# Kernel tuning notes

Measured on AMD Instinct MI355X. Metric: run time of the kernel, lower is better.

The kernel has to match this reference:

```python
import jax, jax.numpy as jnp
import numpy as np

B, T, TQ, E = 32, 200, 50, 64
P, C = 128, 64
BN_EPS = 1e-6
DICE_EPS = 1e-6


def _bn(x, g, b, m, v):
    # inference-mode batch norm over last axis
    return (x - m) * jax.lax.rsqrt(v + BN_EPS) * g + b


def _dice(x, alpha, m, v):
    # Dice activation: p = sigmoid(BN(x, no scale/shift)); out = p*x + alpha*(1-p)*x
    p = jax.nn.sigmoid((x - m) * jax.lax.rsqrt(v + DICE_EPS))
    return p * x + alpha * (1.0 - p) * x


def setup_inputs() -> dict:
    key = jax.random.key(0)
    ks = jax.random.split(key, 16)
    def g(k, shape, scale=0.05):
        return jax.random.normal(k, shape, dtype=jnp.float32) * scale
    inp = {
        "user_behavior": jax.random.normal(ks[0], (B, T, E), dtype=jnp.float32),
        "items": jax.random.normal(ks[1], (B, TQ, E), dtype=jnp.float32),
        "user_profile": jax.random.normal(ks[2], (B, P), dtype=jnp.float32),
        "context": jax.random.normal(ks[3], (B, C), dtype=jnp.float32),
        # attention MLP
        "W1": g(ks[4], (4 * E, 36)), "b1": jnp.zeros((36,), jnp.float32),
        "dice_alpha": jnp.zeros((36,), jnp.float32),
        "dice_mean": jnp.zeros((36,), jnp.float32),
        "dice_var": jnp.ones((36,), jnp.float32),
        "W2": g(ks[5], (36, 1)), "b2": jnp.zeros((1,), jnp.float32),
        # trunk MLP (input dim E+P+C = 256)
        "bn1_g": jnp.ones((E + P + C,), jnp.float32), "bn1_b": jnp.zeros((E + P + C,), jnp.float32),
        "bn1_m": jnp.zeros((E + P + C,), jnp.float32), "bn1_v": jnp.ones((E + P + C,), jnp.float32),
        "Wm1": g(ks[6], (E + P + C, 256)), "bm1": jnp.zeros((256,), jnp.float32),
        "bn2_g": jnp.ones((256,), jnp.float32), "bn2_b": jnp.zeros((256,), jnp.float32),
        "bn2_m": jnp.zeros((256,), jnp.float32), "bn2_v": jnp.ones((256,), jnp.float32),
        "Wm2": g(ks[7], (256, 128)), "bm2": jnp.zeros((128,), jnp.float32),
        "bn3_g": jnp.ones((128,), jnp.float32), "bn3_b": jnp.zeros((128,), jnp.float32),
        "bn3_m": jnp.zeros((128,), jnp.float32), "bn3_v": jnp.ones((128,), jnp.float32),
        "Wm3": g(ks[8], (128, 64)), "bm3": jnp.zeros((64,), jnp.float32),
    }
    return inp


def reference(user_behavior, items, user_profile, context,
              W1, b1, dice_alpha, dice_mean, dice_var, W2, b2,
              bn1_g, bn1_b, bn1_m, bn1_v, Wm1, bm1,
              bn2_g, bn2_b, bn2_m, bn2_v, Wm2, bm2,
              bn3_g, bn3_b, bn3_m, bn3_v, Wm3, bm3):
    b, t, e = user_behavior.shape
    tq = items.shape[1]
    # tile/concat cross product: (B, T', T, 4E)
    q = jnp.broadcast_to(user_behavior[:, None, :, :], (b, tq, t, e))
    k = jnp.broadcast_to(items[:, :, None, :], (b, tq, t, e))
    x = jnp.concatenate([q, k, q - k, q * k], axis=-1)
    x = jnp.einsum('btsf,fu->btsu', x, W1) + b1
    x = _dice(x, dice_alpha, dice_mean, dice_var)
    weight = (jnp.einsum('btsu,uo->btso', x, W2) + b2)[..., 0]  # (B, T', T)
    # weighted sum over history: (B, T', E)
    interest = jnp.einsum('bts,bse->bte', weight, user_behavior)
    # trunk MLP (dropout is identity at inference)
    up = jnp.broadcast_to(user_profile[:, None, :], (b, tq, user_profile.shape[-1]))
    cx = jnp.broadcast_to(context[:, None, :], (b, tq, context.shape[-1]))
    h = jnp.concatenate([interest, up, cx], axis=-1)
    h = _bn(h, bn1_g, bn1_b, bn1_m, bn1_v)
    h = jax.nn.relu(h @ Wm1 + bm1)
    h = _bn(h, bn2_g, bn2_b, bn2_m, bn2_v)
    h = jax.nn.relu(h @ Wm2 + bm2)
    h = _bn(h, bn3_g, bn3_b, bn3_m, bn3_v)
    h = jax.nn.relu(h @ Wm3 + bm3)
    return h
```

## Files before the change

### kernel.cpp

```cpp
#include <hip/hip_runtime.h>
#include <hip/hip_bf16.h>
#include <math.h>

#define NB  32
#define NT  200
#define NTQ 50
#define NE  64
#define NP  128
#define NC  64
#define NU  36
#define NROW (NB * NTQ)

typedef __attribute__((ext_vector_type(8))) short bf8;
typedef __attribute__((ext_vector_type(4))) float f4;

#define WM1F_OFF 0
#define WM2F_OFF 65536
#define WM3F_OFF 98304
#define W1F_OFF  106496
#define HH_OFF   115712

#define ATTN_BLOCKS 1600
#define PACK_ELEMS  (65536 + 32768 + 8192)
#define PACK_BLOCKS (PACK_ELEMS / 256)

__device__ __forceinline__ short f2bf(float x) {
    __hip_bfloat16 h = __float2bfloat16(x);
    return __builtin_bit_cast(short, h);
}
__device__ __forceinline__ float bf2f(short s) {
    unsigned u = ((unsigned)(unsigned short)s) << 16;
    return __builtin_bit_cast(float, u);
}

__global__ __launch_bounds__(256) void prep_w1(const float* __restrict__ W1,
                                               short* __restrict__ w1f) {
    int j = blockIdx.x * 256 + threadIdx.x;
    int i = j & 7, lane = (j >> 3) & 63, tile = j >> 9;
    int ks = tile % 6, nt = tile / 6;
    int kk = ks * 32 + 8 * (lane >> 4) + i;
    int n  = nt * 16 + (lane & 15);
    float v = 0.f;
    if (n < NU) {
        if (kk < 128) {
            v = W1[(128 + kk) * NU + n];
            if (kk < 64) v += W1[kk * NU + n];
        } else {
            v = W1[(kk - 64) * NU + n] - W1[kk * NU + n];
        }
    }
    w1f[j] = f2bf(v);
}

__device__ __forceinline__ void pack_frag(int j, const float* W, int N, int ksc, short* dst) {
    int i    = j & 7;
    int lane = (j >> 3) & 63;
    int tile = j >> 9;
    int ks = tile % ksc;
    int nt = tile / ksc;
    int k = ks * 32 + 8 * (lane >> 4) + i;
    int n = nt * 16 + (lane & 15);
    dst[j] = f2bf(W[k * N + n]);
}

struct AParams {
    const float *ub, *it, *b1, *W2, *b2, *da, *dm, *dv;
    const float *bn1_g, *bn1_b, *bn1_m, *bn1_v;
    const float *Wm1, *Wm2, *Wm3;
    const short *w1f;
    short *wm1f, *wm2f, *wm3f;
    short* Hh;
};

__global__ __launch_bounds__(256) void attn(AParams P) {
    const int bid = blockIdx.x;
    const int tid = threadIdx.x;

    if (bid >= ATTN_BLOCKS) {
        int j = (bid - ATTN_BLOCKS) * 256 + tid;
        if (j < 65536) { pack_frag(j, P.Wm1, 256, 8, P.wm1f); return; }
        j -= 65536;
        if (j < 32768) { pack_frag(j, P.Wm2, 128, 8, P.wm2f); return; }
        j -= 32768;
        pack_frag(j, P.Wm3, 64, 4, P.wm3f);
        return;
    }

    __shared__ float w_s[NT];
    __shared__ float red_s[256];

    const int l = tid & 63, w = tid >> 6;
    const int tq = bid % NTQ, b = bid / NTQ;
    const int ul = l & 15;

    const bf8* wf = (const bf8*)P.w1f;

    bf8 bfr[3][4];
    #pragma unroll
    for (int nt = 0; nt < 3; ++nt)
        #pragma unroll
        for (int ks = 0; ks < 4; ++ks)
            bfr[nt][ks] = wf[(nt * 6 + ks) * 64 + l];

    bf8 ak[2];
    {
        const float* itr = P.it + ((size_t)b * NTQ + tq) * NE;
        #pragma unroll
        for (int ks = 0; ks < 2; ++ks) {
            int e0 = ks * 32 + 8 * (l >> 4);
            f4 v0 = *(const f4*)(itr + e0);
            f4 v1 = *(const f4*)(itr + e0 + 4);
            #pragma unroll
            for (int i = 0; i < 4; ++i) {
                ak[ks][i]     = f2bf(v0[i]);
                ak[ks][4 + i] = f2bf(v1[i]);
            }
        }
    }

    f4 acc0[3];
    #pragma unroll
    for (int nt = 0; nt < 3; ++nt) {
        bf8 kb0 = wf[(nt * 6 + 4) * 64 + l];
        bf8 kb1 = wf[(nt * 6 + 5) * 64 + l];
        f4 z; z[0]=0.f; z[1]=0.f; z[2]=0.f; z[3]=0.f;
        z = __builtin_amdgcn_mfma_f32_16x16x32_bf16(ak[0], kb0, z, 0, 0, 0);
        z = __builtin_amdgcn_mfma_f32_16x16x32_bf16(ak[1], kb1, z, 0, 0, 0);
        acc0[nt] = z;
    }

    float b1v[3], dmv[3], drs[3], dav[3], w2v[3];
    #pragma unroll
    for (int nt = 0; nt < 3; ++nt) {
        int u = nt * 16 + ul;
        bool v = (u < NU);
        int uc = v ? u : (NU - 1);
        b1v[nt] = P.b1[uc];
        dmv[nt] = P.dm[uc];
        drs[nt] = rsqrtf(P.dv[uc] + 1e-6f);
        dav[nt] = P.da[uc];
        w2v[nt] = v ? P.W2[uc] : 0.f;
    }
    const float b2s = P.b2[0];

    for (int tt = w; tt < 13; tt += 4) {
        const int t0 = tt * 16;
        const int tA = t0 + (l & 15);

        bf8 aq[2], ap[2];
        if (tA < NT) {
            const float* ubr = P.ub + ((size_t)b * NT + tA) * NE;
            #pragma unroll
            for (int ks = 0; ks < 2; ++ks) {
                int e0 = ks * 32 + 8 * (l >> 4);
                f4 u0 = *(const f4*)(ubr + e0);
                f4 u1 = *(const f4*)(ubr + e0 + 4);
                #pragma unroll
                for (int i = 0; i < 4; ++i) {
                    float q0 = u0[i], q1 = u1[i];
                    aq[ks][i]     = f2bf(q0);
                    aq[ks][4 + i] = f2bf(q1);
                    ap[ks][i]     = f2bf(q0 * bf2f(ak[ks][i]));
                    ap[ks][4 + i] = f2bf(q1 * bf2f(ak[ks][4 + i]));
                }
            }
        } else {
            #pragma unroll
            for (int ks = 0; ks < 2; ++ks)
                #pragma unroll
                for (int i = 0; i < 8; ++i) { aq[ks][i] = 0; ap[ks][i] = 0; }
        }

        f4 acc[3];
        #pragma unroll
        for (int nt = 0; nt < 3; ++nt) acc[nt] = acc0[nt];
        #pragma unroll
        for (int nt = 0; nt < 3; ++nt) {
            acc[nt] = __builtin_amdgcn_mfma_f32_16x16x32_bf16(aq[0], bfr[nt][0], acc[nt], 0, 0, 0);
            acc[nt] = __builtin_amdgcn_mfma_f32_16x16x32_bf16(aq[1], bfr[nt][1], acc[nt], 0, 0, 0);
            acc[nt] = __builtin_amdgcn_mfma_f32_16x16x32_bf16(ap[0], bfr[nt][2], acc[nt], 0, 0, 0);
            acc[nt] = __builtin_amdgcn_mfma_f32_16x16x32_bf16(ap[1], bfr[nt][3], acc[nt], 0, 0, 0);
        }

        const int tD = t0 + 4 * (l >> 4);
        #pragma unroll
        for (int i = 0; i < 4; ++i) {
            int t = tD + i;
            bool tv = (t < NT);
            float val = 0.f;
            #pragma unroll
            for (int nt = 0; nt < 3; ++nt) {
                float x = acc[nt][i] + b1v[nt];
                float z = (x - dmv[nt]) * drs[nt];
                float p = 1.f / (1.f + __expf(-z));
                val += x * (dav[nt] + p * (1.f - dav[nt])) * w2v[nt];
            }
            val += __shfl_xor(val, 1);
            val += __shfl_xor(val, 2);
            val += __shfl_xor(val, 4);
            val += __shfl_xor(val, 8);
            if (ul == 0 && tv) w_s[t] = val + b2s;
        }
    }
    __syncthreads();

    {
        const int e = tid & 63, g = tid >> 6;
        const float* ubb = P.ub + (size_t)b * NT * NE;
        float s = 0.f;
        #pragma unroll 5
        for (int t = g * 50; t < g * 50 + 50; ++t)
            s = fmaf(w_s[t], ubb[t * NE + e], s);
        red_s[tid] = s;
    }
    __syncthreads();
    if (tid < 64) {
        float tot = red_s[tid] + red_s[64 + tid] + red_s[128 + tid] + red_s[192 + tid];
        float hn = (tot - P.bn1_m[tid]) * rsqrtf(P.bn1_v[tid] + 1e-6f) * P.bn1_g[tid] + P.bn1_b[tid];
        P.Hh[((size_t)b * NTQ + tq) * 64 + tid] = f2bf(hn);
    }
}

struct TParams {
    const short *Hh, *wm1f, *wm2f, *wm3f;
    const float *up, *cx;
    const float *bn1_g, *bn1_b, *bn1_m, *bn1_v;
    const float *bm1, *bm2, *bm3;
    const float *bn2_g, *bn2_b, *bn2_m, *bn2_v;
    const float *bn3_g, *bn3_b, *bn3_m, *bn3_v;
    float* out;
};

#define LSTR 264

__global__ __launch_bounds__(256) void trunk(TParams P) {
    __shared__ short Ha[16 * LSTR];
    __shared__ short Hb[16 * LSTR];

    const int tid = threadIdx.x;
    const int l = tid & 63, w = tid >> 6;
    const int row0 = blockIdx.x * 16;

    {
        const bf8* src = (const bf8*)(P.Hh + (size_t)row0 * 64);
        for (int ch = tid; ch < 16 * 8; ch += 256) {
            int r = ch >> 3, c8 = ch & 7;
            *(bf8*)&Ha[r * LSTR + c8 * 8] = src[r * 8 + c8];
        }
    }
    for (int ch = tid; ch < 16 * 192; ch += 256) {
        int r = ch / 192, c = ch % 192;
        int col = 64 + c;
        int b = (row0 + r) / NTQ;
        float val = (c < NP) ? P.up[b * NP + c] : P.cx[b * NC + (c - NP)];
        float hn = (val - P.bn1_m[col]) * rsqrtf(P.bn1_v[col] + 1e-6f)
                   * P.bn1_g[col] + P.bn1_b[col];
        Ha[r * LSTR + col] = f2bf(hn);
    }
    __syncthreads();

    const int ar = l & 15;
    const int rl = 4 * (l >> 4);
    const int nl = l & 15;

    {
        bf8 a[8];
        #pragma unroll
        for (int ks = 0; ks < 8; ++ks)
            a[ks] = *(const bf8*)&Ha[ar * LSTR + ks * 32 + 8 * (l >> 4)];
        const bf8* wf = (const bf8*)P.wm1f;
        #pragma unroll
        for (int nt0 = 0; nt0 < 4; ++nt0) {
            int nt = w * 4 + nt0;
            f4 acc; acc[0]=0.f; acc[1]=0.f; acc[2]=0.f; acc[3]=0.f;
            #pragma unroll
            for (int ks = 0; ks < 8; ++ks)
                acc = __builtin_amdgcn_mfma_f32_16x16x32_bf16(a[ks], wf[(nt * 8 + ks) * 64 + l], acc, 0, 0, 0);
            int n = nt * 16 + nl;
            float g1 = P.bn2_g[n] * rsqrtf(P.bn2_v[n] + 1e-6f);
            float c1 = P.bn2_b[n] - P.bn2_m[n] * g1;
            float bias = P.bm1[n];
            #pragma unroll
            for (int i = 0; i < 4; ++i) {
                float v = fmaxf(acc[i] + bias, 0.f);
                Hb[(rl + i) * LSTR + n] = f2bf(v * g1 + c1);
            }
        }
    }
    __syncthreads();

    {
        bf8 a[8];
        #pragma unroll
        for (int ks = 0; ks < 8; ++ks)
            a[ks] = *(const bf8*)&Hb[ar * LSTR + ks * 32 + 8 * (l >> 4)];
        const bf8* wf = (const bf8*)P.wm2f;
        #pragma unroll
        for (int nt0 = 0; nt0 < 2; ++nt0) {
            int nt = w * 2 + nt0;
            f4 acc; acc[0]=0.f; acc[1]=0.f; acc[2]=0.f; acc[3]=0.f;
            #pragma unroll
            for (int ks = 0; ks < 8; ++ks)
                acc = __builtin_amdgcn_mfma_f32_16x16x32_bf16(a[ks], wf[(nt * 8 + ks) * 64 + l], acc, 0, 0, 0);
            int n = nt * 16 + nl;
            float g1 = P.bn3_g[n] * rsqrtf(P.bn3_v[n] + 1e-6f);
            float c1 = P.bn3_b[n] - P.bn3_m[n] * g1;
            float bias = P.bm2[n];
            #pragma unroll
            for (int i = 0; i < 4; ++i) {
                float v = fmaxf(acc[i] + bias, 0.f);
                Ha[(rl + i) * LSTR + n] = f2bf(v * g1 + c1);
            }
        }
    }
    __syncthreads();

    {
        bf8 a[4];
        #pragma unroll
        for (int ks = 0; ks < 4; ++ks)
            a[ks] = *(const bf8*)&Ha[ar * LSTR + ks * 32 + 8 * (l >> 4)];
        const bf8* wf = (const bf8*)P.wm3f;
        {
            int nt = w;
            f4 acc; acc[0]=0.f; acc[1]=0.f; acc[2]=0.f; acc[3]=0.f;
            #pragma unroll
            for (int ks = 0; ks < 4; ++ks)
                acc = __builtin_amdgcn_mfma_f32_16x16x32_bf16(a[ks], wf[(nt * 4 + ks) * 64 + l], acc, 0, 0, 0);
            int n = nt * 16 + nl;
            float bias = P.bm3[n];
            #pragma unroll
            for (int i = 0; i < 4; ++i)
                P.out[(size_t)(row0 + rl + i) * 64 + n] = fmaxf(acc[i] + bias, 0.f);
        }
    }
}

extern "C" void kernel_launch(void* const* d_in, const int* in_sizes, int n_in,
                              void* d_out, int out_size, void* d_ws, size_t ws_size,
                              hipStream_t stream) {
    (void)in_sizes; (void)n_in; (void)out_size; (void)ws_size;

    const float* ub         = (const float*)d_in[0];
    const float* it         = (const float*)d_in[1];
    const float* up         = (const float*)d_in[2];
    const float* cx         = (const float*)d_in[3];
    const float* W1         = (const float*)d_in[4];
    const float* b1         = (const float*)d_in[5];
    const float* dice_alpha = (const float*)d_in[6];
    const float* dice_mean  = (const float*)d_in[7];
    const float* dice_var   = (const float*)d_in[8];
    const float* W2         = (const float*)d_in[9];
    const float* b2         = (const float*)d_in[10];
    const float* bn1_g      = (const float*)d_in[11];
    const float* bn1_b      = (const float*)d_in[12];
    const float* bn1_m      = (const float*)d_in[13];
    const float* bn1_v      = (const float*)d_in[14];
    const float* Wm1        = (const float*)d_in[15];
    const float* bm1        = (const float*)d_in[16];
    const float* bn2_g      = (const float*)d_in[17];
    const float* bn2_b      = (const float*)d_in[18];
    const float* bn2_m      = (const float*)d_in[19];
    const float* bn2_v      = (const float*)d_in[20];
    const float* Wm2        = (const float*)d_in[21];
    const float* bm2        = (const float*)d_in[22];
    const float* bn3_g      = (const float*)d_in[23];
    const float* bn3_b      = (const float*)d_in[24];
    const float* bn3_m      = (const float*)d_in[25];
    const float* bn3_v      = (const float*)d_in[26];
    const float* Wm3        = (const float*)d_in[27];
    const float* bm3        = (const float*)d_in[28];

    short* wsb  = (short*)d_ws;
    short* wm1f = wsb + WM1F_OFF;
    short* wm2f = wsb + WM2F_OFF;
    short* wm3f = wsb + WM3F_OFF;
    short* w1f  = wsb + W1F_OFF;
    short* Hh   = wsb + HH_OFF;

    prep_w1<<<36, 256, 0, stream>>>(W1, w1f);

    AParams A;
    A.ub = ub; A.it = it; A.b1 = b1;
    A.W2 = W2; A.b2 = b2; A.da = dice_alpha; A.dm = dice_mean; A.dv = dice_var;
    A.bn1_g = bn1_g; A.bn1_b = bn1_b; A.bn1_m = bn1_m; A.bn1_v = bn1_v;
    A.Wm1 = Wm1; A.Wm2 = Wm2; A.Wm3 = Wm3;
    A.w1f = w1f; A.wm1f = wm1f; A.wm2f = wm2f; A.wm3f = wm3f;
    A.Hh = Hh;
    attn<<<ATTN_BLOCKS + PACK_BLOCKS, 256, 0, stream>>>(A);

    TParams T;
    T.Hh = Hh; T.wm1f = wm1f; T.wm2f = wm2f; T.wm3f = wm3f;
    T.up = up; T.cx = cx;
    T.bn1_g = bn1_g; T.bn1_b = bn1_b; T.bn1_m = bn1_m; T.bn1_v = bn1_v;
    T.bm1 = bm1; T.bm2 = bm2; T.bm3 = bm3;
    T.bn2_g = bn2_g; T.bn2_b = bn2_b; T.bn2_m = bn2_m; T.bn2_v = bn2_v;
    T.bn3_g = bn3_g; T.bn3_b = bn3_b; T.bn3_m = bn3_m; T.bn3_v = bn3_v;
    T.out = (float*)d_out;
    trunk<<<NROW / 16, 256, 0, stream>>>(T);
}
```

Measured before the change: 149.4 us.

## Precompute item projection in fp32, regrid attention by history tile, move interest sum into trunk

The item-side projection (k·(W1_k − W1_diff) + b1) is now computed once per query row in fp32 by the prep kernel, so the attention MFMA K-dimension drops from 192 to 128. The attention grid is reorganised to one block per (batch, 16-history tile), with each wave looping over the 50 queries. That lets the behaviour fragment be loaded once and reused, and the raw weights are written to a global buffer. The weighted sum over history plus the first batch norm move into the trunk kernel, which reads the weights into LDS. This adds a global round-trip for the weight matrix and a heavier trunk prologue, in exchange for fewer, denser attention blocks.

Measured after the change: 158.0 us. 5.8% more time.

```diff
diff --git a/kernel.cpp b/kernel.cpp
--- a/kernel.cpp
+++ b/kernel.cpp
@@ -12,15 +12,17 @@
 #define NROW (NB * NTQ)
 
 typedef __attribute__((ext_vector_type(8))) short bf8;
+typedef __attribute__((ext_vector_type(4))) short s4v;
 typedef __attribute__((ext_vector_type(4))) float f4;
 
 #define WM1F_OFF 0
 #define WM2F_OFF 65536
 #define WM3F_OFF 98304
 #define W1F_OFF  106496
-#define HH_OFF   115712
-
-#define ATTN_BLOCKS 1600
+#define KW_BYTE  225280
+#define W_BYTE   455680
+
+#define ATTN_BLOCKS 416
 #define PACK_ELEMS  (65536 + 32768 + 8192)
 #define PACK_BLOCKS (PACK_ELEMS / 256)
 
@@ -33,23 +35,33 @@
     return __builtin_bit_cast(float, u);
 }
 
-__global__ __launch_bounds__(256) void prep_w1(const float* __restrict__ W1,
-                                               short* __restrict__ w1f) {
-    int j = blockIdx.x * 256 + threadIdx.x;
-    int i = j & 7, lane = (j >> 3) & 63, tile = j >> 9;
-    int ks = tile % 6, nt = tile / 6;
+__global__ __launch_bounds__(256) void prep(
+    const float* __restrict__ it, const float* __restrict__ W1,
+    const float* __restrict__ b1,
+    float* __restrict__ kW, short* __restrict__ w1f)
+{
+    int idx = blockIdx.x * 256 + threadIdx.x;
+    if (idx < NROW * NU) {
+        int u = idx % NU, row = idx / NU;
+        const float* k = it + row * NE;
+        float acc = b1[u];
+        #pragma unroll 4
+        for (int e = 0; e < NE; ++e)
+            acc = fmaf(k[e], W1[(64 + e) * NU + u] - W1[(128 + e) * NU + u], acc);
+        kW[idx] = acc;
+        return;
+    }
+    idx -= NROW * NU;
+    int i = idx & 7, lane = (idx >> 3) & 63, tile = idx >> 9;
+    int ks = tile & 3, nt = tile >> 2;
     int kk = ks * 32 + 8 * (lane >> 4) + i;
     int n  = nt * 16 + (lane & 15);
     float v = 0.f;
     if (n < NU) {
-        if (kk < 128) {
-            v = W1[(128 + kk) * NU + n];
-            if (kk < 64) v += W1[kk * NU + n];
-        } else {
-            v = W1[(kk - 64) * NU + n] - W1[kk * NU + n];
-        }
-    }
-    w1f[j] = f2bf(v);
+        v = W1[(128 + kk) * NU + n];
+        if (kk < 64) v += W1[kk * NU + n];
+    }
+    w1f[idx] = f2bf(v);
 }
 
 __device__ __forceinline__ void pack_frag(int j, const float* W, int N, int ksc, short* dst) {
@@ -64,15 +76,14 @@
 }
 
 struct AParams {
-    const float *ub, *it, *b1, *W2, *b2, *da, *dm, *dv;
-    const float *bn1_g, *bn1_b, *bn1_m, *bn1_v;
+    const float *ub, *it, *kW, *W2, *b2, *da, *dm, *dv;
     const float *Wm1, *Wm2, *Wm3;
     const short *w1f;
     short *wm1f, *wm2f, *wm3f;
-    short* Hh;
+    float *w;
 };
 
-__global__ __launch_bounds__(256) void attn(AParams P) {
+__global__ __launch_bounds__(256) void attn2(AParams P) {
     const int bid = blockIdx.x;
     const int tid = threadIdx.x;
 
@@ -86,94 +97,77 @@
         return;
     }
 
-    __shared__ float w_s[NT];
-    __shared__ float red_s[256];
-
-    const int l = tid & 63, w = tid >> 6;
-    const int tq = bid % NTQ, b = bid / NTQ;
+    const int l = tid & 63, wv = tid >> 6;
+    const int tt = bid % 13, b = bid / 13;
+    const int t0 = tt * 16;
     const int ul = l & 15;
 
     const bf8* wf = (const bf8*)P.w1f;
-
     bf8 bfr[3][4];
     #pragma unroll
     for (int nt = 0; nt < 3; ++nt)
         #pragma unroll
         for (int ks = 0; ks < 4; ++ks)
-            bfr[nt][ks] = wf[(nt * 6 + ks) * 64 + l];
-
-    bf8 ak[2];
-    {
-        const float* itr = P.it + ((size_t)b * NTQ + tq) * NE;
+            bfr[nt][ks] = wf[(nt * 4 + ks) * 64 + l];
+
+    int tA = t0 + ul; if (tA > NT - 1) tA = NT - 1;
+    bf8 aq[2];
+    {
+        const float* ubr = P.ub + ((size_t)b * NT + tA) * NE;
         #pragma unroll
         for (int ks = 0; ks < 2; ++ks) {
             int e0 = ks * 32 + 8 * (l >> 4);
-            f4 v0 = *(const f4*)(itr + e0);
-            f4 v1 = *(const f4*)(itr + e0 + 4);
+            f4 u0 = *(const f4*)(ubr + e0);
+            f4 u1 = *(const f4*)(ubr + e0 + 4);
             #pragma unroll
             for (int i = 0; i < 4; ++i) {
-                ak[ks][i]     = f2bf(v0[i]);
-                ak[ks][4 + i] = f2bf(v1[i]);
+                aq[ks][i]     = f2bf(u0[i]);
+                aq[ks][4 + i] = f2bf(u1[i]);
             }
         }
     }
 
-    f4 acc0[3];
-    #pragma unroll
-    for (int nt = 0; nt < 3; ++nt) {
-        bf8 kb0 = wf[(nt * 6 + 4) * 64 + l];
-        bf8 kb1 = wf[(nt * 6 + 5) * 64 + l];
-        f4 z; z[0]=0.f; z[1]=0.f; z[2]=0.f; z[3]=0.f;
-        z = __builtin_amdgcn_mfma_f32_16x16x32_bf16(ak[0], kb0, z, 0, 0, 0);
-        z = __builtin_amdgcn_mfma_f32_16x16x32_bf16(ak[1], kb1, z, 0, 0, 0);
-        acc0[nt] = z;
-    }
-
-    float b1v[3], dmv[3], drs[3], dav[3], w2v[3];
+    float dmv[3], drs[3], dav[3], w2v[3];
     #pragma unroll
     for (int nt = 0; nt < 3; ++nt) {
         int u = nt * 16 + ul;
         bool v = (u < NU);
         int uc = v ? u : (NU - 1);
-        b1v[nt] = P.b1[uc];
         dmv[nt] = P.dm[uc];
         drs[nt] = rsqrtf(P.dv[uc] + 1e-6f);
         dav[nt] = P.da[uc];
         w2v[nt] = v ? P.W2[uc] : 0.f;
     }
     const float b2s = P.b2[0];
-
-    for (int tt = w; tt < 13; tt += 4) {
-        const int t0 = tt * 16;
-        const int tA = t0 + (l & 15);
-
-        bf8 aq[2], ap[2];
-        if (tA < NT) {
-            const float* ubr = P.ub + ((size_t)b * NT + tA) * NE;
+    const float* kwb = P.kW + (size_t)b * NTQ * NU;
+    const float* itb = P.it + (size_t)b * NTQ * NE;
+
+    for (int tq = wv; tq < NTQ; tq += 4) {
+        bf8 ap[2];
+        {
+            const float* itr = itb + tq * NE;
             #pragma unroll
             for (int ks = 0; ks < 2; ++ks) {
                 int e0 = ks * 32 + 8 * (l >> 4);
-                f4 u0 = *(const f4*)(ubr + e0);
-                f4 u1 = *(const f4*)(ubr + e0 + 4);
+                f4 v0 = *(const f4*)(itr + e0);
+                f4 v1 = *(const f4*)(itr + e0 + 4);
                 #pragma unroll
                 for (int i = 0; i < 4; ++i) {
-                    float q0 = u0[i], q1 = u1[i];
-                    aq[ks][i]     = f2bf(q0);
-                    aq[ks][4 + i] = f2bf(q1);
-                    ap[ks][i]     = f2bf(q0 * bf2f(ak[ks][i]));
-                    ap[ks][4 + i] = f2bf(q1 * bf2f(ak[ks][4 + i]));
+                    ap[ks][i]     = f2bf(bf2f(aq[ks][i])     * v0[i]);
+                    ap[ks][4 + i] = f2bf(bf2f(aq[ks][4 + i]) * v1[i]);
                 }
             }
-        } else {
-            #pragma unroll
-            for (int ks = 0; ks < 2; ++ks)
-                #pragma unroll
-                for (int i = 0; i < 8; ++i) { aq[ks][i] = 0; ap[ks][i] = 0; }
+        }
+        float kwv[3];
+        #pragma unroll
+        for (int nt = 0; nt < 3; ++nt) {
+            int u = nt * 16 + ul;
+            kwv[nt] = kwb[tq * NU + ((u < NU) ? u : (NU - 1))];
         }
 
         f4 acc[3];
         #pragma unroll
-        for (int nt = 0; nt < 3; ++nt) acc[nt] = acc0[nt];
+        for (int nt = 0; nt < 3; ++nt) { acc[nt][0]=0.f; acc[nt][1]=0.f; acc[nt][2]=0.f; acc[nt][3]=0.f; }
         #pragma unroll
         for (int nt = 0; nt < 3; ++nt) {
             acc[nt] = __builtin_amdgcn_mfma_f32_16x16x32_bf16(aq[0], bfr[nt][0], acc[nt], 0, 0, 0);
@@ -182,48 +176,39 @@
             acc[nt] = __builtin_amdgcn_mfma_f32_16x16x32_bf16(ap[1], bfr[nt][3], acc[nt], 0, 0, 0);
         }
 
-        const int tD = t0 + 4 * (l >> 4);
+        float val[4];
         #pragma unroll
         for (int i = 0; i < 4; ++i) {
-            int t = tD + i;
-            bool tv = (t < NT);
-            float val = 0.f;
+            float s = 0.f;
             #pragma unroll
             for (int nt = 0; nt < 3; ++nt) {
-                float x = acc[nt][i] + b1v[nt];
+                float x = acc[nt][i] + kwv[nt];
                 float z = (x - dmv[nt]) * drs[nt];
                 float p = 1.f / (1.f + __expf(-z));
-                val += x * (dav[nt] + p * (1.f - dav[nt])) * w2v[nt];
+                s += x * (dav[nt] + p * (1.f - dav[nt])) * w2v[nt];
             }
-            val += __shfl_xor(val, 1);
-            val += __shfl_xor(val, 2);
-            val += __shfl_xor(val, 4);
-            val += __shfl_xor(val, 8);
-            if (ul == 0 && tv) w_s[t] = val + b2s;
-        }
-    }
-    __syncthreads();
-
-    {
-        const int e = tid & 63, g = tid >> 6;
-        const float* ubb = P.ub + (size_t)b * NT * NE;
-        float s = 0.f;
-        #pragma unroll 5
-        for (int t = g * 50; t < g * 50 + 50; ++t)
-            s = fmaf(w_s[t], ubb[t * NE + e], s);
-        red_s[tid] = s;
-    }
-    __syncthreads();
-    if (tid < 64) {
-        float tot = red_s[tid] + red_s[64 + tid] + red_s[128 + tid] + red_s[192 + tid];
-        float hn = (tot - P.bn1_m[tid]) * rsqrtf(P.bn1_v[tid] + 1e-6f) * P.bn1_g[tid] + P.bn1_b[tid];
-        P.Hh[((size_t)b * NTQ + tq) * 64 + tid] = f2bf(hn);
+            val[i] = s;
+        }
+        #pragma unroll
+        for (int i = 0; i < 4; ++i) {
+            val[i] += __shfl_xor(val[i], 1);
+            val[i] += __shfl_xor(val[i], 2);
+            val[i] += __shfl_xor(val[i], 4);
+            val[i] += __shfl_xor(val[i], 8);
+        }
+        int trow = t0 + 4 * (l >> 4);
+        if (ul == 0 && trow < NT) {
+            f4 o;
+            o[0] = val[0] + b2s; o[1] = val[1] + b2s;
+            o[2] = val[2] + b2s; o[3] = val[3] + b2s;
+            *(f4*)&P.w[((size_t)b * NTQ + tq) * NT + trow] = o;
+        }
     }
 }
 
 struct TParams {
-    const short *Hh, *wm1f, *wm2f, *wm3f;
-    const float *up, *cx;
+    const float *w, *ub, *up, *cx;
+    const short *wm1f, *wm2f, *wm3f;
     const float *bn1_g, *bn1_b, *bn1_m, *bn1_v;
     const float *bm1, *bm2, *bm3;
     const float *bn2_g, *bn2_b, *bn2_m, *bn2_v;
@@ -232,8 +217,10 @@
 };
 
 #define LSTR 264
+#define WSTR 204
 
 __global__ __launch_bounds__(256) void trunk(TParams P) {
+    __shared__ float w_s[16 * WSTR];
     __shared__ short Ha[16 * LSTR];
     __shared__ short Hb[16 * LSTR];
 
@@ -242,11 +229,39 @@
     const int row0 = blockIdx.x * 16;
 
     {
-        const bf8* src = (const bf8*)(P.Hh + (size_t)row0 * 64);
-        for (int ch = tid; ch < 16 * 8; ch += 256) {
-            int r = ch >> 3, c8 = ch & 7;
-            *(bf8*)&Ha[r * LSTR + c8 * 8] = src[r * 8 + c8];
-        }
+        const f4* src = (const f4*)(P.w + (size_t)row0 * NT);
+        for (int ch = tid; ch < 800; ch += 256) {
+            int t = ch * 4;
+            int r = t / NT, c = t - r * NT;
+            *(f4*)&w_s[r * WSTR + c] = src[ch];
+        }
+    }
+    __syncthreads();
+
+    {
+        int r  = tid >> 4;
+        int e4 = (tid & 15) * 4;
+        int bb = (row0 + r) / NTQ;
+        const f4* ub4 = (const f4*)(P.ub + (size_t)bb * NT * NE + e4);
+        f4 s; s[0]=0.f; s[1]=0.f; s[2]=0.f; s[3]=0.f;
+        #pragma unroll 8
+        for (int t = 0; t < NT; ++t) {
+            float wt = w_s[r * WSTR + t];
+            f4 u = ub4[(size_t)t * (NE / 4)];
+            s[0] = fmaf(wt, u[0], s[0]);
+            s[1] = fmaf(wt, u[1], s[1]);
+            s[2] = fmaf(wt, u[2], s[2]);
+            s[3] = fmaf(wt, u[3], s[3]);
+        }
+        s4v hv;
+        #pragma unroll
+        for (int j = 0; j < 4; ++j) {
+            int col = e4 + j;
+            float hn = (s[j] - P.bn1_m[col]) * rsqrtf(P.bn1_v[col] + 1e-6f)
+                       * P.bn1_g[col] + P.bn1_b[col];
+            hv[j] = f2bf(hn);
+        }
+        *(s4v*)&Ha[r * LSTR + e4] = hv;
     }
     for (int ch = tid; ch < 16 * 192; ch += 256) {
         int r = ch / 192, c = ch % 192;
@@ -376,22 +391,23 @@
     short* wm2f = wsb + WM2F_OFF;
     short* wm3f = wsb + WM3F_OFF;
     short* w1f  = wsb + W1F_OFF;
-    short* Hh   = wsb + HH_OFF;
-
-    prep_w1<<<36, 256, 0, stream>>>(W1, w1f);
+    float* kW   = (float*)((char*)d_ws + KW_BYTE);
+    float* wbuf = (float*)((char*)d_ws + W_BYTE);
+
+    const int prep_total = NROW * NU + 6144;
+    prep<<<(prep_total + 255) / 256, 256, 0, stream>>>(it, W1, b1, kW, w1f);
 
     AParams A;
-    A.ub = ub; A.it = it; A.b1 = b1;
+    A.ub = ub; A.it = it; A.kW = kW;
     A.W2 = W2; A.b2 = b2; A.da = dice_alpha; A.dm = dice_mean; A.dv = dice_var;
-    A.bn1_g = bn1_g; A.bn1_b = bn1_b; A.bn1_m = bn1_m; A.bn1_v = bn1_v;
     A.Wm1 = Wm1; A.Wm2 = Wm2; A.Wm3 = Wm3;
     A.w1f = w1f; A.wm1f = wm1f; A.wm2f = wm2f; A.wm3f = wm3f;
-    A.Hh = Hh;
-    attn<<<ATTN_BLOCKS + PACK_BLOCKS, 256, 0, stream>>>(A);
+    A.w = wbuf;
+    attn2<<<ATTN_BLOCKS + PACK_BLOCKS, 256, 0, stream>>>(A);
 
     TParams T;
-    T.Hh = Hh; T.wm1f = wm1f; T.wm2f = wm2f; T.wm3f = wm3f;
-    T.up = up; T.cx = cx;
+    T.w = wbuf; T.ub = ub; T.up = up; T.cx = cx;
+    T.wm1f = wm1f; T.wm2f = wm2f; T.wm3f = wm3f;
     T.bn1_g = bn1_g; T.bn1_b = bn1_b; T.bn1_m = bn1_m; T.bn1_v = bn1_v;
     T.bm1 = bm1; T.bm2 = bm2; T.bm3 = bm3;
     T.bn2_g = bn2_g; T.bn2_b = bn2_b; T.bn2_m = bn2_m; T.bn2_v = bn2_v;
```
